# Kernel tuning notes

Measured on AMD Instinct MI355X. Metric: run time of the kernel, lower is better.

Reference implementation:

```python
import jax, jax.numpy as jnp
import numpy as np

B, N, D = 4, 2048, 1024
H, DH = 16, 64
MAX_POS_EMB = 256
TOPK = 64


def setup_inputs() -> dict:
    key = jax.random.key(0)
    ks = jax.random.split(key, 8)
    s = 0.02
    inner = H * DH
    return {
        "x": jax.random.normal(ks[0], (B, N, D), jnp.float32),
        "gating_mask": jax.random.uniform(ks[1], (B, 1, N, 1), jnp.float32),
        "Wq": jax.random.normal(ks[2], (D, inner), jnp.float32) * s,
        "bq": jnp.zeros((inner,), jnp.float32),
        "Wkv": jax.random.normal(ks[3], (D, 2 * inner), jnp.float32) * s,
        "bkv": jnp.zeros((2 * inner,), jnp.float32),
        "Wo": jax.random.normal(ks[4], (inner, D), jnp.float32) * s,
        "bo": jnp.zeros((D,), jnp.float32),
        "rel_emb": jax.random.normal(ks[5], (MAX_POS_EMB, DH), jnp.float32) * s,
        "mask": jnp.ones((B, N), bool),
        "sparse_topk": TOPK,
    }


def reference(x, gating_mask, Wq, bq, Wkv, bkv, Wo, bo, rel_emb, mask, sparse_topk):
    b, n, d = x.shape
    h, dh = H, DH
    scale = dh ** -0.5
    mask_val = -jnp.finfo(x.dtype).max

    # projections -> [b, h, n, dh]
    q = (x @ Wq + bq).reshape(b, n, h, dh).transpose(0, 2, 1, 3)
    kv = x @ Wkv + bkv
    k = kv[..., : h * dh].reshape(b, n, h, dh).transpose(0, 2, 1, 3)
    v = kv[..., h * dh:].reshape(b, n, h, dh).transpose(0, 2, 1, 3)

    dots = jnp.einsum("bhid,bhjd->bhij", q, k) * scale  # [b,h,n,n]

    # relative positional bias: q . E[clip(i-j+M, 0, M-1)]
    seq = jnp.arange(n)
    dist = jnp.clip(seq[:, None] - seq[None, :] + MAX_POS_EMB, 0, MAX_POS_EMB - 1)
    qE = jnp.einsum("bhid,rd->bhir", q, rel_emb) * scale  # [b,h,n,R]
    pos_attn = jnp.take_along_axis(qE, dist[None, None, :, :], axis=-1)  # [b,h,n,n]
    dots = dots + pos_attn

    # padding mask: mask_i * mask_j
    full_mask = mask[:, None, :, None] & mask[:, None, None, :]
    dots = jnp.where(full_mask, dots, mask_val)

    # topk sparsification: keep only scores >= k-th largest per row
    top = jax.lax.top_k(dots, sparse_topk)[0]  # [b,h,n,topk]
    vk = top[..., -1:]
    dots = jnp.where(dots < vk, mask_val, dots)

    attn = jax.nn.softmax(dots, axis=-1)
    attn = attn * gating_mask

    out = jnp.einsum("bhij,bhjd->bhid", attn, v)
    out = out.transpose(0, 2, 1, 3).reshape(b, n, h * dh)
    return out @ Wo + bo
```

## Files before the change

kernel.cpp:

```cpp
#include <hip/hip_runtime.h>
#include <stdint.h>


typedef __attribute__((ext_vector_type(8))) short short8;
typedef __attribute__((ext_vector_type(4))) float floatx4;

#define Bn   4
#define Nn   2048
#define Hn   16
#define BHn  (Bn*Hn)
#define DELTA 0.00125f

__device__ __forceinline__ float bf2f(unsigned short u) {
  union { unsigned int i; float f; } v; v.i = ((unsigned int)u) << 16; return v.f;
}
__device__ __forceinline__ unsigned short f2bf(float f) {
  union { float f; unsigned int i; } v; v.f = f;
  unsigned int r = v.i + 0x7fffu + ((v.i >> 16) & 1u);
  return (unsigned short)(r >> 16);
}
__device__ __forceinline__ floatx4 mfma16(short8 a, short8 b, floatx4 c) {
  return __builtin_amdgcn_mfma_f32_16x16x32_bf16(a, b, c, 0, 0, 0);
}
__device__ __forceinline__ void split2(float x, unsigned short& h, unsigned short& m) {
  h = f2bf(x);
  m = f2bf(x - bf2f(h));
}
__device__ __forceinline__ void split3(float x, unsigned short& h, unsigned short& m, unsigned short& l) {
  h = f2bf(x);
  float r = x - bf2f(h);
  m = f2bf(r);
  l = f2bf(r - bf2f(m));
}

__global__ __launch_bounds__(256)
void transpose_split3(const float* __restrict__ W,
                      unsigned short* __restrict__ T0,
                      unsigned short* __restrict__ T1,
                      unsigned short* __restrict__ T2,
                      int K, int Ncols)
{
  __shared__ float tile[32][33];
  int k0 = blockIdx.y * 32, n0 = blockIdx.x * 32;
  int tx = threadIdx.x & 31, ty = threadIdx.x >> 5;
  for (int s = 0; s < 32; s += 8)
    tile[ty + s][tx] = W[(size_t)(k0 + ty + s) * Ncols + n0 + tx];
  __syncthreads();
  for (int s = 0; s < 32; s += 8) {
    float x = tile[tx][ty + s];
    unsigned short h, m, l;
    split3(x, h, m, l);
    size_t o = (size_t)(n0 + ty + s) * K + k0 + tx;
    T0[o] = h; T1[o] = m; T2[o] = l;
  }
}

__global__ __launch_bounds__(256)
void transpose_split2(const float* __restrict__ W,
                      unsigned short* __restrict__ T0,
                      unsigned short* __restrict__ T1,
                      int K, int Ncols)
{
  __shared__ float tile[32][33];
  int k0 = blockIdx.y * 32, n0 = blockIdx.x * 32;
  int tx = threadIdx.x & 31, ty = threadIdx.x >> 5;
  for (int s = 0; s < 32; s += 8)
    tile[ty + s][tx] = W[(size_t)(k0 + ty + s) * Ncols + n0 + tx];
  __syncthreads();
  for (int s = 0; s < 32; s += 8) {
    float x = tile[tx][ty + s];
    unsigned short h, m;
    split2(x, h, m);
    size_t o = (size_t)(n0 + ty + s) * K + k0 + tx;
    T0[o] = h; T1[o] = m;
  }
}

__global__ __launch_bounds__(256)
void convert_bf16(const float* __restrict__ in, unsigned short* __restrict__ outp, int n) {
  int i = blockIdx.x * 256 + threadIdx.x;
  if (i < n) outp[i] = f2bf(in[i]);
}

__global__ __launch_bounds__(256)
void gemm_qkv(const float* __restrict__ A,
              const unsigned short* __restrict__ B0,
              const unsigned short* __restrict__ B1,
              const unsigned short* __restrict__ B2,
              const float* __restrict__ bias,
              float* __restrict__ O32,
              unsigned short* __restrict__ Oh,
              unsigned short* __restrict__ Om,
              _Float16* __restrict__ Vh,
              int K, float scale)
{
  __shared__ unsigned short lA[3][128 * 40];
  __shared__ unsigned short lB[3][128 * 40];
  const int tid = threadIdx.x;
  const int lane = tid & 63;
  const int m0 = blockIdx.y * 128, n0 = blockIdx.x * 128;
  const bool vblk = (n0 >= 1024);
  const int wid = tid >> 6, wm = wid >> 1, wn = wid & 1;
  const int fr = lane & 15, fq = lane >> 4;
  floatx4 acc[4][4] = {};

  for (int k0 = 0; k0 < K; k0 += 32) {
    __syncthreads();
    #pragma unroll
    for (int p = 0; p < 2; p++) {
      int c = tid + p * 256;
      int row = c >> 2, kc = (c & 3) * 8;
      size_t go = (size_t)(m0 + row) * K + k0 + kc;
      float4 v0 = *(const float4*)&A[go];
      float4 v1 = *(const float4*)&A[go + 4];
      union { unsigned short u[8]; uint4 q; } hh, mm, ll;
      float xs[8] = {v0.x, v0.y, v0.z, v0.w, v1.x, v1.y, v1.z, v1.w};
      #pragma unroll
      for (int e = 0; e < 8; e++) split3(xs[e], hh.u[e], mm.u[e], ll.u[e]);
      *(uint4*)&lA[0][row * 40 + kc] = hh.q;
      *(uint4*)&lA[1][row * 40 + kc] = mm.q;
      size_t bo = (size_t)(n0 + row) * K + k0 + kc;
      *(uint4*)&lB[0][row * 40 + kc] = *(const uint4*)&B0[bo];
      *(uint4*)&lB[1][row * 40 + kc] = *(const uint4*)&B1[bo];
      if (!vblk) {
        *(uint4*)&lA[2][row * 40 + kc] = ll.q;
        *(uint4*)&lB[2][row * 40 + kc] = *(const uint4*)&B2[bo];
      }
    }
    __syncthreads();
    short8 af0[4], af1[4], af2[4], bf0[4], bf1[4], bf2v[4];
    #pragma unroll
    for (int t = 0; t < 4; t++) {
      int ao = (wm * 64 + t * 16 + fr) * 40 + 8 * fq;
      int bo2 = (wn * 64 + t * 16 + fr) * 40 + 8 * fq;
      af0[t] = *(const short8*)&lA[0][ao];
      af1[t] = *(const short8*)&lA[1][ao];
      bf0[t] = *(const short8*)&lB[0][bo2];
      bf1[t] = *(const short8*)&lB[1][bo2];
      if (!vblk) {
        af2[t] = *(const short8*)&lA[2][ao];
        bf2v[t] = *(const short8*)&lB[2][bo2];
      }
    }
    #pragma unroll
    for (int mi = 0; mi < 4; mi++)
      #pragma unroll
      for (int ni = 0; ni < 4; ni++) {
        acc[mi][ni] = mfma16(af0[mi], bf0[ni], acc[mi][ni]);
        acc[mi][ni] = mfma16(af0[mi], bf1[ni], acc[mi][ni]);
        acc[mi][ni] = mfma16(af1[mi], bf0[ni], acc[mi][ni]);
        if (!vblk) {
          acc[mi][ni] = mfma16(af1[mi], bf1[ni], acc[mi][ni]);
          acc[mi][ni] = mfma16(af0[mi], bf2v[ni], acc[mi][ni]);
          acc[mi][ni] = mfma16(af2[mi], bf0[ni], acc[mi][ni]);
        }
      }
  }
  #pragma unroll
  for (int mi = 0; mi < 4; mi++)
    #pragma unroll
    for (int ni = 0; ni < 4; ni++) {
      int nl = n0 + wn * 64 + ni * 16 + fr;
      float bv = bias[nl];
      #pragma unroll
      for (int rg = 0; rg < 4; rg++) {
        int ml = m0 + wm * 64 + mi * 16 + fq * 4 + rg;
        float val = (acc[mi][ni][rg] + bv) * scale;
        int bb = ml >> 11, ii = ml & 2047;
        int hh2 = (nl & 1023) >> 6, dd = nl & 63;
        size_t idx = (((size_t)bb * Hn + hh2) * Nn + ii) * 64 + dd;
        if (!vblk) {
          O32[idx] = val;
          unsigned short h, m;
          split2(val, h, m);
          Oh[idx] = h; Om[idx] = m;
        } else {
          Vh[idx] = (_Float16)val;
        }
      }
    }
}

__global__ __launch_bounds__(256)
void gemm_out(const float* __restrict__ A,
              const unsigned short* __restrict__ B0,
              const unsigned short* __restrict__ B1,
              const float* __restrict__ bias,
              float* __restrict__ O32,
              int Ncols, int K)
{
  __shared__ unsigned short lA[2][128 * 40];
  __shared__ unsigned short lB[2][128 * 40];
  const int tid = threadIdx.x;
  const int lane = tid & 63;
  const int m0 = blockIdx.y * 128, n0 = blockIdx.x * 128;
  const int wid = tid >> 6, wm = wid >> 1, wn = wid & 1;
  const int fr = lane & 15, fq = lane >> 4;
  floatx4 acc[4][4] = {};

  for (int k0 = 0; k0 < K; k0 += 32) {
    __syncthreads();
    #pragma unroll
    for (int p = 0; p < 2; p++) {
      int c = tid + p * 256;
      int row = c >> 2, kc = (c & 3) * 8;
      size_t go = (size_t)(m0 + row) * K + k0 + kc;
      float4 v0 = *(const float4*)&A[go];
      float4 v1 = *(const float4*)&A[go + 4];
      union { unsigned short u[8]; uint4 q; } hh, mm;
      float xs[8] = {v0.x, v0.y, v0.z, v0.w, v1.x, v1.y, v1.z, v1.w};
      #pragma unroll
      for (int e = 0; e < 8; e++) split2(xs[e], hh.u[e], mm.u[e]);
      *(uint4*)&lA[0][row * 40 + kc] = hh.q;
      *(uint4*)&lA[1][row * 40 + kc] = mm.q;
      size_t bo = (size_t)(n0 + row) * K + k0 + kc;
      *(uint4*)&lB[0][row * 40 + kc] = *(const uint4*)&B0[bo];
      *(uint4*)&lB[1][row * 40 + kc] = *(const uint4*)&B1[bo];
    }
    __syncthreads();
    short8 af[2][4], bfr[2][4];
    #pragma unroll
    for (int s = 0; s < 2; s++)
      #pragma unroll
      for (int t = 0; t < 4; t++) {
        af[s][t]  = *(const short8*)&lA[s][(wm * 64 + t * 16 + fr) * 40 + 8 * fq];
        bfr[s][t] = *(const short8*)&lB[s][(wn * 64 + t * 16 + fr) * 40 + 8 * fq];
      }
    #pragma unroll
    for (int mi = 0; mi < 4; mi++)
      #pragma unroll
      for (int ni = 0; ni < 4; ni++) {
        acc[mi][ni] = mfma16(af[0][mi], bfr[0][ni], acc[mi][ni]);
        acc[mi][ni] = mfma16(af[0][mi], bfr[1][ni], acc[mi][ni]);
        acc[mi][ni] = mfma16(af[1][mi], bfr[0][ni], acc[mi][ni]);
      }
  }
  #pragma unroll
  for (int mi = 0; mi < 4; mi++)
    #pragma unroll
    for (int ni = 0; ni < 4; ni++) {
      int nl = n0 + wn * 64 + ni * 16 + fr;
      float bv = bias[nl];
      #pragma unroll
      for (int rg = 0; rg < 4; rg++) {
        int ml = m0 + wm * 64 + mi * 16 + fq * 4 + rg;
        O32[(size_t)ml * Ncols + nl] = acc[mi][ni][rg] + bv;
      }
    }
}

__global__ __launch_bounds__(1024, 8)
void attn_k(const unsigned short* __restrict__ qh,
            const unsigned short* __restrict__ qm,
            const unsigned short* __restrict__ kh,
            const unsigned short* __restrict__ km,
            const _Float16* __restrict__ vh,
            const float* __restrict__ q32,
            const float* __restrict__ k32,
            const unsigned short* __restrict__ relbf,
            const float* __restrict__ rel32,
            const float* __restrict__ gating,
            const int* __restrict__ topkp,
            float* __restrict__ inner)
{
  extern __shared__ char smem[];
  _Float16* S = (_Float16*)smem;
  unsigned short* KtH = (unsigned short*)(smem + 65536);
  unsigned short* KtM = KtH + 4096;
  _Float16* qE = (_Float16*)KtH;

  const int ib = blockIdx.x, bh = blockIdx.y;
  const int i0 = ib * 16;
  const int b = bh >> 4, h = bh & 15;
  const int tid = threadIdx.x;
  const int lane = tid & 63, w = tid >> 6;
  const int fr = lane & 15, fq = lane >> 4;
  const int topk = topkp[0];

  const size_t qoff = ((size_t)bh * Nn + i0) * 64;
  const size_t qf = qoff + (size_t)fr * 64 + 8 * fq;
  const short8 aqh0 = *(const short8*)&qh[qf];
  const short8 aqh1 = *(const short8*)&qh[qf + 32];
  const short8 aqm0 = *(const short8*)&qm[qf];
  const short8 aqm1 = *(const short8*)&qm[qf + 32];

  for (int jt = 0; jt < 32; jt++) {
    __syncthreads();
    {
      int sel = tid >> 9;
      int row = (tid >> 3) & 63, ch = tid & 7;
      int dst = row * 64 + ((ch ^ (row & 7)) * 8);
      size_t g = ((size_t)bh * Nn + jt * 64 + row) * 64 + ch * 8;
      unsigned short* T = sel ? KtM : KtH;
      const unsigned short* src = sel ? km : kh;
      *(uint4*)&T[dst] = *(const uint4*)&src[g];
    }
    __syncthreads();
    if (w < 8 && ((jt & 1) == (w >> 2))) {
      int wc = w & 3;
      int row16 = wc * 16 + fr, r7 = fr & 7;
      int b0 = row16 * 64 + ((fq ^ r7) * 8);
      int b1 = row16 * 64 + (((fq + 4) ^ r7) * 8);
      short8 kh0 = *(const short8*)&KtH[b0];
      short8 kh1 = *(const short8*)&KtH[b1];
      short8 km0 = *(const short8*)&KtM[b0];
      short8 km1 = *(const short8*)&KtM[b1];
      floatx4 c = {};
      c = mfma16(aqh0, kh0, c); c = mfma16(aqh1, kh1, c);
      c = mfma16(aqh0, km0, c); c = mfma16(aqh1, km1, c);
      c = mfma16(aqm0, kh0, c); c = mfma16(aqm1, kh1, c);
      int colsw = jt * 64 + ((wc ^ fq) * 16) + fr;
      #pragma unroll
      for (int rg = 0; rg < 4; rg++)
        S[(fq * 4 + rg) * 2048 + colsw] = (_Float16)c[rg];
    }
  }
  __syncthreads();

  {
    size_t rf = (size_t)(w * 16 + fr) * 64 + 8 * fq;
    short8 rb0 = *(const short8*)&relbf[rf];
    short8 rb1 = *(const short8*)&relbf[rf + 32];
    floatx4 c = {};
    c = mfma16(aqh0, rb0, c); c = mfma16(aqh1, rb1, c);
    c = mfma16(aqm0, rb0, c); c = mfma16(aqm1, rb1, c);
    int colsw = ((w ^ fq) * 16) + fr;
    #pragma unroll
    for (int rg = 0; rg < 4; rg++)
      qE[(fq * 4 + rg) * 256 + colsw] = (_Float16)c[rg];
  }
  __syncthreads();

  const int r = w;
  const int i = i0 + r;
  const int X = (r >> 2) << 4;
  _Float16* S0 = S + r * 2048;
  const _Float16* qE0 = qE + r * 256;
  const float cA = (float)qE0[255 ^ X], cC = (float)qE0[X];
  const int swl = (2 * lane) ^ X;

  float key[32];
  float mx = -3.0e38f, sm = 0.f, sq = 0.f;
  #pragma unroll
  for (int e = 0; e < 16; e++) {
    const int jb = 128 * e;
    union { unsigned int u; _Float16 hx[2]; } u0;
    u0.u = *(const unsigned int*)&S0[jb + swl];
    const int j0 = jb + 2 * lane;
    float e0, e1;
    if (jb + 127 <= i) { e0 = cA; e1 = cA; }
    else if (jb >= i + 256) { e0 = cC; e1 = cC; }
    else {
      int c0 = i - j0 + 256; c0 = c0 < 0 ? 0 : (c0 > 255 ? 255 : c0);
      int c1 = i - j0 + 255; c1 = c1 < 0 ? 0 : (c1 > 255 ? 255 : c1);
      e0 = (float)qE0[c0 ^ X]; e1 = (float)qE0[c1 ^ X];
    }
    float a0 = (float)u0.hx[0] + e0, a1 = (float)u0.hx[1] + e1;
    key[2 * e] = a0; key[2 * e + 1] = a1;
    mx = fmaxf(mx, fmaxf(a0, a1));
    sm += a0 + a1;
    sq = fmaf(a0, a0, fmaf(a1, a1, sq));
  }
  #pragma unroll
  for (int d = 1; d < 64; d <<= 1) {
    mx = fmaxf(mx, __shfl_xor(mx, d));
    sm += __shfl_xor(sm, d);
    sq += __shfl_xor(sq, d);
  }
  const float mu = sm * (1.f / 2048.f);
  const float sg = sqrtf(fmaxf(sq * (1.f / 2048.f) - mu * mu, 0.f)) + 1e-9f;

  auto cntGE = [&](float u) -> int {
    int c = 0;
    #pragma unroll
    for (int t = 0; t < 32; t++) c += (key[t] >= u) ? 1 : 0;
    #pragma unroll
    for (int d = 1; d < 64; d <<= 1) c += __shfl_xor(c, d);
    return c;
  };

  float lo = mu + 1.6f * sg;
  float hi = mx + fabsf(mx) * 1e-6f + 1e-20f;
  if (cntGE(lo) < topk) {
    lo = mu;
    if (cntGE(lo) < topk) lo = mu - 20.f * sg;
  }
  #pragma unroll 1
  for (int it = 0; it < 10; it++) {
    float mid = 0.5f * (lo + hi);
    if (cntGE(mid) >= topk) lo = mid; else hi = mid;
  }
  const float C = hi + 2.f * DELTA, L = lo - 2.f * DELTA;

  char* sb = (char*)S0;
  float* Pl = (float*)sb;          int* Jl = (int*)(sb + 512);
  float* Sx = (float*)(sb + 1024); int* Jc = (int*)(sb + 1280);
  asm volatile("" ::: "memory");
  const unsigned long long lmlt = (1ull << lane) - 1ull;

  int base = 0, mc = 0;
  #pragma unroll
  for (int t = 0; t < 32; t++) {
    const int j = 2 * lane + 128 * (t >> 1) + (t & 1);
    bool dk = key[t] >= C;
    bool cd = (key[t] >= L) && !dk;
    unsigned long long mk = __ballot(dk);
    if (dk) { int pos = base + __popcll(mk & lmlt); Pl[pos] = key[t]; Jl[pos] = j; }
    base += __popcll(mk);
    mk = __ballot(cd);
    if (cd) { int pos = mc + __popcll(mk & lmlt); if (pos < 64) Jc[pos] = j; }
    mc += __popcll(mk);
  }
  if (mc > 64) mc = 64;
  asm volatile("" ::: "memory");

  const double qv = (double)q32[((size_t)bh * Nn + i) * 64 + lane];
  #pragma unroll 1
  for (int c2 = 0; c2 < mc; c2++) {
    int j = Jc[c2];
    int ridx = i - j + 256; ridx = ridx < 0 ? 0 : (ridx > 255 ? 255 : ridx);
    double t = qv * ((double)k32[((size_t)bh * Nn + j) * 64 + lane] +
                     (double)rel32[ridx * 64 + lane]);
    #pragma unroll
    for (int d = 1; d < 64; d <<= 1) t += __shfl_xor(t, d);
    if (lane == 0) Sx[c2] = (float)t;
  }
  asm volatile("" ::: "memory");

  const int need = topk - base;
  float myx = (lane < mc) ? Sx[lane] : -3.0e38f;
  int rank = 0;
  #pragma unroll 1
  for (int c2 = 0; c2 < mc; c2++) {
    float o = Sx[c2];
    rank += (o > myx || (o == myx && c2 < lane)) ? 1 : 0;
  }
  unsigned long long bm = __ballot((lane < mc) && (rank == need - 1));
  float vk = bm ? __shfl(myx, (int)__ffsll(bm) - 1) : 3.0e38f;
  bool ck = (lane < mc) && ((rank < need) || (myx == vk));
  unsigned long long km2 = __ballot(ck);
  if (ck) { int pos = base + __popcll(km2 & lmlt); Pl[pos] = myx; Jl[pos] = Jc[lane]; }
  const int nk = base + __popcll(km2);
  asm volatile("" ::: "memory");

  float ps = 0.f;
  #pragma unroll 1
  for (int t = lane; t < nk; t += 64) { float p = __expf(Pl[t] - mx); Pl[t] = p; ps += p; }
  #pragma unroll
  for (int d = 1; d < 64; d <<= 1) ps += __shfl_xor(ps, d);
  const float coef = gating[(size_t)b * Nn + i] / ps;
  asm volatile("" ::: "memory");

  const _Float16* vbp = vh + (size_t)bh * Nn * 64 + lane;
  float a0 = 0.f, a1 = 0.f, a2 = 0.f, a3 = 0.f;
  int t4 = nk & ~3;
  #pragma unroll 1
  for (int t = 0; t < t4; t += 4) {
    float p0 = Pl[t], p1 = Pl[t + 1], p2 = Pl[t + 2], p3 = Pl[t + 3];
    int j0 = Jl[t], j1 = Jl[t + 1], j2 = Jl[t + 2], j3 = Jl[t + 3];
    a0 += p0 * (float)vbp[(size_t)j0 * 64];
    a1 += p1 * (float)vbp[(size_t)j1 * 64];
    a2 += p2 * (float)vbp[(size_t)j2 * 64];
    a3 += p3 * (float)vbp[(size_t)j3 * 64];
  }
  #pragma unroll 1
  for (int t = t4; t < nk; t++) a0 += Pl[t] * (float)vbp[(size_t)Jl[t] * 64];
  inner[((size_t)b * Nn + i) * 1024 + h * 64 + lane] = (a0 + a1 + a2 + a3) * coef;
}

extern "C" void kernel_launch(void* const* d_in, const int* in_sizes, int n_in,
                              void* d_out, int out_size, void* d_ws, size_t ws_size,
                              hipStream_t stream) {
  const float* x      = (const float*)d_in[0];
  const float* gating = (const float*)d_in[1];
  const float* Wq     = (const float*)d_in[2];
  const float* bq     = (const float*)d_in[3];
  const float* Wkv    = (const float*)d_in[4];
  const float* bkv    = (const float*)d_in[5];
  const float* Wo     = (const float*)d_in[6];
  const float* bo     = (const float*)d_in[7];
  const float* rel    = (const float*)d_in[8];
  const int*   topk   = (const int*)d_in[10];
  float* out = (float*)d_out;

  char* ws = (char*)d_ws;
  size_t off = 0;
  auto alloc = [&](size_t bytes) -> void* {
    void* p = ws + off; off += (bytes + 255) & ~(size_t)255; return p;
  };
  unsigned short* Wqt0 = (unsigned short*)alloc(1024ull * 1024 * 2);
  unsigned short* Wqt1 = (unsigned short*)alloc(1024ull * 1024 * 2);
  unsigned short* Wqt2 = (unsigned short*)alloc(1024ull * 1024 * 2);
  unsigned short* Wkt0 = (unsigned short*)alloc(2048ull * 1024 * 2);
  unsigned short* Wkt1 = (unsigned short*)alloc(2048ull * 1024 * 2);
  unsigned short* Wkt2 = (unsigned short*)alloc(2048ull * 1024 * 2);
  unsigned short* Wot0 = (unsigned short*)alloc(1024ull * 1024 * 2);
  unsigned short* Wot1 = (unsigned short*)alloc(1024ull * 1024 * 2);
  unsigned short* relbf = (unsigned short*)alloc(256ull * 64 * 2);
  float* q32 = (float*)alloc((size_t)BHn * Nn * 64 * 4);
  float* k32 = (float*)alloc((size_t)BHn * Nn * 64 * 4);
  unsigned short* qhb = (unsigned short*)alloc((size_t)BHn * Nn * 64 * 2);
  unsigned short* qmb = (unsigned short*)alloc((size_t)BHn * Nn * 64 * 2);
  unsigned short* khb = (unsigned short*)alloc((size_t)BHn * Nn * 64 * 2);
  unsigned short* kmb = (unsigned short*)alloc((size_t)BHn * Nn * 64 * 2);
  _Float16* vhb = (_Float16*)alloc((size_t)BHn * Nn * 64 * 2);
  float* inner = (float*)alloc((size_t)Bn * Nn * 1024 * 4);
  if (off > ws_size) return;

  size_t shmem = 65536 + 16384;
  (void)hipFuncSetAttribute((const void*)attn_k,
                            hipFuncAttributeMaxDynamicSharedMemorySize, (int)shmem);

  transpose_split3<<<dim3(32, 32), 256, 0, stream>>>(Wq, Wqt0, Wqt1, Wqt2, 1024, 1024);
  transpose_split3<<<dim3(64, 32), 256, 0, stream>>>(Wkv, Wkt0, Wkt1, Wkt2, 1024, 2048);
  transpose_split2<<<dim3(32, 32), 256, 0, stream>>>(Wo, Wot0, Wot1, 1024, 1024);
  convert_bf16<<<dim3(64), 256, 0, stream>>>(rel, relbf, 256 * 64);

  gemm_qkv<<<dim3(8, 64), 256, 0, stream>>>(x, Wqt0, Wqt1, Wqt2, bq,
      q32, qhb, qmb, vhb, 1024, 0.125f);
  gemm_qkv<<<dim3(16, 64), 256, 0, stream>>>(x, Wkt0, Wkt1, Wkt2, bkv,
      k32, khb, kmb, vhb, 1024, 1.0f);

  attn_k<<<dim3(128, 64), 1024, shmem, stream>>>(qhb, qmb, khb, kmb, vhb,
      q32, k32, relbf, rel, gating, topk, inner);

  gemm_out<<<dim3(8, 64), 256, 0, stream>>>(inner, Wot0, Wot1, bo,
      out, 1024, 1024);
}
```

Measured before the change: 1.174 ms.

## Presplit GEMM inputs into bf16 limbs and use integer-coded top-k threshold search

Adds a presplit kernel so x is split into three bf16 limbs once, rather than inside every GEMM tile load. q/k fp32 copies are replaced by three-limb bf16 outputs, and attention writes bf16 hi/lo limbs for the output GEMM. The top-k threshold search now runs a bisection over order-preserving fp16 integer codes packed two per register instead of float keys with mean/std bracketing. Index and code are packed together in shared memory, and the candidate margin DELTA is widened. This cuts register use and repeated conversion work, at the cost of an extra pass over x and coarser fp16-quantized keys.

New measurement: 1.365 ms. +16.2%, slower.

```diff
diff --git a/kernel.cpp b/kernel.cpp
--- a/kernel.cpp
+++ b/kernel.cpp
@@ -9,7 +9,7 @@
 #define Nn   2048
 #define Hn   16
 #define BHn  (Bn*Hn)
-#define DELTA 0.00125f
+#define DELTA 0.002f
 
 __device__ __forceinline__ float bf2f(unsigned short u) {
   union { unsigned int i; float f; } v; v.i = ((unsigned int)u) << 16; return v.f;
@@ -31,6 +31,36 @@
   float r = x - bf2f(h);
   m = f2bf(r);
   l = f2bf(r - bf2f(m));
+}
+__device__ __forceinline__ unsigned int map16(unsigned int b) {
+  return (b & 0x8000u) ? (b ^ 0xFFFFu) : (b | 0x8000u);
+}
+__device__ __forceinline__ unsigned int mapf(float f) {
+  union { _Float16 h; unsigned short s; } u; u.h = (_Float16)f;
+  return map16((unsigned int)u.s);
+}
+__device__ __forceinline__ float unmapf(unsigned int c) {
+  unsigned int b = (c & 0x8000u) ? (c ^ 0x8000u) : (c ^ 0xFFFFu);
+  union { _Float16 h; unsigned short s; } u; u.s = (unsigned short)b;
+  return (float)u.h;
+}
+
+__global__ __launch_bounds__(256)
+void presplit3(const float* __restrict__ x,
+               unsigned short* __restrict__ H,
+               unsigned short* __restrict__ M,
+               unsigned short* __restrict__ L, int n4)
+{
+  int i = blockIdx.x * 256 + threadIdx.x;
+  if (i >= n4) return;
+  float4 v = ((const float4*)x)[i];
+  union { unsigned short u[4]; uint2 q; } hh, mm, ll;
+  float xs[4] = {v.x, v.y, v.z, v.w};
+  #pragma unroll
+  for (int e = 0; e < 4; e++) split3(xs[e], hh.u[e], mm.u[e], ll.u[e]);
+  ((uint2*)H)[i] = hh.q;
+  ((uint2*)M)[i] = mm.q;
+  ((uint2*)L)[i] = ll.q;
 }
 
 __global__ __launch_bounds__(256)
@@ -83,14 +113,16 @@
 }
 
 __global__ __launch_bounds__(256)
-void gemm_qkv(const float* __restrict__ A,
+void gemm_qkv(const unsigned short* __restrict__ Ah,
+              const unsigned short* __restrict__ Am,
+              const unsigned short* __restrict__ Al,
               const unsigned short* __restrict__ B0,
               const unsigned short* __restrict__ B1,
               const unsigned short* __restrict__ B2,
               const float* __restrict__ bias,
-              float* __restrict__ O32,
               unsigned short* __restrict__ Oh,
               unsigned short* __restrict__ Om,
+              unsigned short* __restrict__ Ol,
               _Float16* __restrict__ Vh,
               int K, float scale)
 {
@@ -111,19 +143,13 @@
       int c = tid + p * 256;
       int row = c >> 2, kc = (c & 3) * 8;
       size_t go = (size_t)(m0 + row) * K + k0 + kc;
-      float4 v0 = *(const float4*)&A[go];
-      float4 v1 = *(const float4*)&A[go + 4];
-      union { unsigned short u[8]; uint4 q; } hh, mm, ll;
-      float xs[8] = {v0.x, v0.y, v0.z, v0.w, v1.x, v1.y, v1.z, v1.w};
-      #pragma unroll
-      for (int e = 0; e < 8; e++) split3(xs[e], hh.u[e], mm.u[e], ll.u[e]);
-      *(uint4*)&lA[0][row * 40 + kc] = hh.q;
-      *(uint4*)&lA[1][row * 40 + kc] = mm.q;
+      *(uint4*)&lA[0][row * 40 + kc] = *(const uint4*)&Ah[go];
+      *(uint4*)&lA[1][row * 40 + kc] = *(const uint4*)&Am[go];
       size_t bo = (size_t)(n0 + row) * K + k0 + kc;
       *(uint4*)&lB[0][row * 40 + kc] = *(const uint4*)&B0[bo];
       *(uint4*)&lB[1][row * 40 + kc] = *(const uint4*)&B1[bo];
       if (!vblk) {
-        *(uint4*)&lA[2][row * 40 + kc] = ll.q;
+        *(uint4*)&lA[2][row * 40 + kc] = *(const uint4*)&Al[go];
         *(uint4*)&lB[2][row * 40 + kc] = *(const uint4*)&B2[bo];
       }
     }
@@ -170,10 +196,9 @@
         int hh2 = (nl & 1023) >> 6, dd = nl & 63;
         size_t idx = (((size_t)bb * Hn + hh2) * Nn + ii) * 64 + dd;
         if (!vblk) {
-          O32[idx] = val;
-          unsigned short h, m;
-          split2(val, h, m);
-          Oh[idx] = h; Om[idx] = m;
+          unsigned short h, m, l;
+          split3(val, h, m, l);
+          Oh[idx] = h; Om[idx] = m; Ol[idx] = l;
         } else {
           Vh[idx] = (_Float16)val;
         }
@@ -182,7 +207,8 @@
 }
 
 __global__ __launch_bounds__(256)
-void gemm_out(const float* __restrict__ A,
+void gemm_out(const unsigned short* __restrict__ Ah,
+              const unsigned short* __restrict__ Am,
               const unsigned short* __restrict__ B0,
               const unsigned short* __restrict__ B1,
               const float* __restrict__ bias,
@@ -205,14 +231,8 @@
       int c = tid + p * 256;
       int row = c >> 2, kc = (c & 3) * 8;
       size_t go = (size_t)(m0 + row) * K + k0 + kc;
-      float4 v0 = *(const float4*)&A[go];
-      float4 v1 = *(const float4*)&A[go + 4];
-      union { unsigned short u[8]; uint4 q; } hh, mm;
-      float xs[8] = {v0.x, v0.y, v0.z, v0.w, v1.x, v1.y, v1.z, v1.w};
-      #pragma unroll
-      for (int e = 0; e < 8; e++) split2(xs[e], hh.u[e], mm.u[e]);
-      *(uint4*)&lA[0][row * 40 + kc] = hh.q;
-      *(uint4*)&lA[1][row * 40 + kc] = mm.q;
+      *(uint4*)&lA[0][row * 40 + kc] = *(const uint4*)&Ah[go];
+      *(uint4*)&lA[1][row * 40 + kc] = *(const uint4*)&Am[go];
       size_t bo = (size_t)(n0 + row) * K + k0 + kc;
       *(uint4*)&lB[0][row * 40 + kc] = *(const uint4*)&B0[bo];
       *(uint4*)&lB[1][row * 40 + kc] = *(const uint4*)&B1[bo];
@@ -252,16 +272,17 @@
 __global__ __launch_bounds__(1024, 8)
 void attn_k(const unsigned short* __restrict__ qh,
             const unsigned short* __restrict__ qm,
+            const unsigned short* __restrict__ ql,
             const unsigned short* __restrict__ kh,
             const unsigned short* __restrict__ km,
+            const unsigned short* __restrict__ kl,
             const _Float16* __restrict__ vh,
-            const float* __restrict__ q32,
-            const float* __restrict__ k32,
             const unsigned short* __restrict__ relbf,
             const float* __restrict__ rel32,
             const float* __restrict__ gating,
             const int* __restrict__ topkp,
-            float* __restrict__ inner)
+            unsigned short* __restrict__ innerh,
+            unsigned short* __restrict__ innerm)
 {
   extern __shared__ char smem[];
   _Float16* S = (_Float16*)smem;
@@ -339,8 +360,8 @@
   const float cA = (float)qE0[255 ^ X], cC = (float)qE0[X];
   const int swl = (2 * lane) ^ X;
 
-  float key[32];
-  float mx = -3.0e38f, sm = 0.f, sq = 0.f;
+  unsigned int kk[16];
+  unsigned int umax = 0;
   #pragma unroll
   for (int e = 0; e < 16; e++) {
     const int jb = 128 * e;
@@ -356,56 +377,58 @@
       e0 = (float)qE0[c0 ^ X]; e1 = (float)qE0[c1 ^ X];
     }
     float a0 = (float)u0.hx[0] + e0, a1 = (float)u0.hx[1] + e1;
-    key[2 * e] = a0; key[2 * e + 1] = a1;
-    mx = fmaxf(mx, fmaxf(a0, a1));
-    sm += a0 + a1;
-    sq = fmaf(a0, a0, fmaf(a1, a1, sq));
-  }
+    unsigned int c0u = mapf(a0), c1u = mapf(a1);
+    kk[e] = c0u | (c1u << 16);
+    unsigned int cmx = c0u > c1u ? c0u : c1u;
+    umax = umax > cmx ? umax : cmx;
+  }
+  unsigned int mxu = umax, mnu = umax;
   #pragma unroll
   for (int d = 1; d < 64; d <<= 1) {
-    mx = fmaxf(mx, __shfl_xor(mx, d));
-    sm += __shfl_xor(sm, d);
-    sq += __shfl_xor(sq, d);
-  }
-  const float mu = sm * (1.f / 2048.f);
-  const float sg = sqrtf(fmaxf(sq * (1.f / 2048.f) - mu * mu, 0.f)) + 1e-9f;
-
-  auto cntGE = [&](float u) -> int {
-    int c = 0;
-    #pragma unroll
-    for (int t = 0; t < 32; t++) c += (key[t] >= u) ? 1 : 0;
-    #pragma unroll
-    for (int d = 1; d < 64; d <<= 1) c += __shfl_xor(c, d);
-    return c;
-  };
-
-  float lo = mu + 1.6f * sg;
-  float hi = mx + fabsf(mx) * 1e-6f + 1e-20f;
-  if (cntGE(lo) < topk) {
-    lo = mu;
-    if (cntGE(lo) < topk) lo = mu - 20.f * sg;
-  }
+    unsigned int o1 = (unsigned int)__shfl_xor((int)mxu, d);
+    unsigned int o2 = (unsigned int)__shfl_xor((int)mnu, d);
+    mxu = o1 > mxu ? o1 : mxu;
+    mnu = o2 < mnu ? o2 : mnu;
+  }
+  const float mxv = unmapf(mxu);
+
+  unsigned int lo = mnu, hi = mxu + 1;
   #pragma unroll 1
-  for (int it = 0; it < 10; it++) {
-    float mid = 0.5f * (lo + hi);
-    if (cntGE(mid) >= topk) lo = mid; else hi = mid;
-  }
-  const float C = hi + 2.f * DELTA, L = lo - 2.f * DELTA;
+  for (int it = 0; it < 13; it++) {
+    unsigned int mid = (lo + hi) >> 1;
+    int cnt = 0;
+    #pragma unroll
+    for (int e = 0; e < 16; e++) {
+      cnt += ((kk[e] & 0xffffu) >= mid) ? 1 : 0;
+      cnt += ((kk[e] >> 16) >= mid) ? 1 : 0;
+    }
+    #pragma unroll
+    for (int d = 1; d < 64; d <<= 1) cnt += __shfl_xor(cnt, d);
+    if (cnt >= topk) lo = mid; else hi = mid;
+  }
+  const float Cv = unmapf(hi) + 2.0f * DELTA;
+  const float Lv = unmapf(lo) - 2.0f * DELTA;
+  const unsigned int Cu = mapf(Cv) + 1;
+  int Lsi = (int)mapf(Lv) - 1;
+  const unsigned int Lu = Lsi < 0 ? 0u : (unsigned int)Lsi;
 
   char* sb = (char*)S0;
-  float* Pl = (float*)sb;          int* Jl = (int*)(sb + 512);
-  float* Sx = (float*)(sb + 1024); int* Jc = (int*)(sb + 1280);
+  unsigned int* Pk = (unsigned int*)sb;
+  int*   Jc = (int*)(sb + 512);
+  float* Sx = (float*)(sb + 768);
+  float* P2 = (float*)(sb + 1024);
   asm volatile("" ::: "memory");
   const unsigned long long lmlt = (1ull << lane) - 1ull;
 
   int base = 0, mc = 0;
   #pragma unroll
   for (int t = 0; t < 32; t++) {
+    unsigned int code = (t & 1) ? (kk[t >> 1] >> 16) : (kk[t >> 1] & 0xffffu);
     const int j = 2 * lane + 128 * (t >> 1) + (t & 1);
-    bool dk = key[t] >= C;
-    bool cd = (key[t] >= L) && !dk;
+    bool dk = code >= Cu;
+    bool cd = (code >= Lu) && !dk;
     unsigned long long mk = __ballot(dk);
-    if (dk) { int pos = base + __popcll(mk & lmlt); Pl[pos] = key[t]; Jl[pos] = j; }
+    if (dk) { int pos = base + __popcll(mk & lmlt); Pk[pos] = (unsigned int)j | (code << 16); }
     base += __popcll(mk);
     mk = __ballot(cd);
     if (cd) { int pos = mc + __popcll(mk & lmlt); if (pos < 64) Jc[pos] = j; }
@@ -414,16 +437,18 @@
   if (mc > 64) mc = 64;
   asm volatile("" ::: "memory");
 
-  const double qv = (double)q32[((size_t)bh * Nn + i) * 64 + lane];
+  const size_t qrow = ((size_t)bh * Nn + i) * 64 + lane;
+  const double qv = (double)bf2f(qh[qrow]) + (double)bf2f(qm[qrow]) + (double)bf2f(ql[qrow]);
   #pragma unroll 1
   for (int c2 = 0; c2 < mc; c2++) {
     int j = Jc[c2];
     int ridx = i - j + 256; ridx = ridx < 0 ? 0 : (ridx > 255 ? 255 : ridx);
-    double t = qv * ((double)k32[((size_t)bh * Nn + j) * 64 + lane] +
-                     (double)rel32[ridx * 64 + lane]);
-    #pragma unroll
-    for (int d = 1; d < 64; d <<= 1) t += __shfl_xor(t, d);
-    if (lane == 0) Sx[c2] = (float)t;
+    size_t krow = ((size_t)bh * Nn + j) * 64 + lane;
+    double kv = (double)bf2f(kh[krow]) + (double)bf2f(km[krow]) + (double)bf2f(kl[krow]);
+    double t2 = qv * (kv + (double)rel32[ridx * 64 + lane]);
+    #pragma unroll
+    for (int d = 1; d < 64; d <<= 1) t2 += __shfl_xor(t2, d);
+    if (lane == 0) Sx[c2] = (float)t2;
   }
   asm volatile("" ::: "memory");
 
@@ -439,13 +464,21 @@
   float vk = bm ? __shfl(myx, (int)__ffsll(bm) - 1) : 3.0e38f;
   bool ck = (lane < mc) && ((rank < need) || (myx == vk));
   unsigned long long km2 = __ballot(ck);
-  if (ck) { int pos = base + __popcll(km2 & lmlt); Pl[pos] = myx; Jl[pos] = Jc[lane]; }
+  float pb = 0.f;
+  if (ck) {
+    int pos = base + __popcll(km2 & lmlt);
+    Pk[pos] = (unsigned int)Jc[lane];
+    pb = __expf(myx - mxv);
+    P2[pos] = pb;
+  }
   const int nk = base + __popcll(km2);
-  asm volatile("" ::: "memory");
-
-  float ps = 0.f;
+  float ps = pb;
   #pragma unroll 1
-  for (int t = lane; t < nk; t += 64) { float p = __expf(Pl[t] - mx); Pl[t] = p; ps += p; }
+  for (int t = lane; t < base; t += 64) {
+    float val = unmapf(Pk[t] >> 16);
+    float p = __expf(val - mxv);
+    P2[t] = p; ps += p;
+  }
   #pragma unroll
   for (int d = 1; d < 64; d <<= 1) ps += __shfl_xor(ps, d);
   const float coef = gating[(size_t)b * Nn + i] / ps;
@@ -456,16 +489,22 @@
   int t4 = nk & ~3;
   #pragma unroll 1
   for (int t = 0; t < t4; t += 4) {
-    float p0 = Pl[t], p1 = Pl[t + 1], p2 = Pl[t + 2], p3 = Pl[t + 3];
-    int j0 = Jl[t], j1 = Jl[t + 1], j2 = Jl[t + 2], j3 = Jl[t + 3];
+    int j0 = (int)(Pk[t] & 0xffffu), j1 = (int)(Pk[t + 1] & 0xffffu);
+    int j2 = (int)(Pk[t + 2] & 0xffffu), j3 = (int)(Pk[t + 3] & 0xffffu);
+    float p0 = P2[t], p1 = P2[t + 1], p2 = P2[t + 2], p3 = P2[t + 3];
     a0 += p0 * (float)vbp[(size_t)j0 * 64];
     a1 += p1 * (float)vbp[(size_t)j1 * 64];
     a2 += p2 * (float)vbp[(size_t)j2 * 64];
     a3 += p3 * (float)vbp[(size_t)j3 * 64];
   }
   #pragma unroll 1
-  for (int t = t4; t < nk; t++) a0 += Pl[t] * (float)vbp[(size_t)Jl[t] * 64];
-  inner[((size_t)b * Nn + i) * 1024 + h * 64 + lane] = (a0 + a1 + a2 + a3) * coef;
+  for (int t = t4; t < nk; t++)
+    a0 += P2[t] * (float)vbp[(size_t)(Pk[t] & 0xffffu) * 64];
+  float outv = (a0 + a1 + a2 + a3) * coef;
+  unsigned short oh, om;
+  split2(outv, oh, om);
+  size_t oidx = ((size_t)b * Nn + i) * 1024 + h * 64 + lane;
+  innerh[oidx] = oh; innerm[oidx] = om;
 }
 
 extern "C" void kernel_launch(void* const* d_in, const int* in_sizes, int n_in,
@@ -497,33 +536,38 @@
   unsigned short* Wot0 = (unsigned short*)alloc(1024ull * 1024 * 2);
   unsigned short* Wot1 = (unsigned short*)alloc(1024ull * 1024 * 2);
   unsigned short* relbf = (unsigned short*)alloc(256ull * 64 * 2);
-  float* q32 = (float*)alloc((size_t)BHn * Nn * 64 * 4);
-  float* k32 = (float*)alloc((size_t)BHn * Nn * 64 * 4);
+  unsigned short* xh = (unsigned short*)alloc(8192ull * 1024 * 2);
+  unsigned short* xm = (unsigned short*)alloc(8192ull * 1024 * 2);
+  unsigned short* xl = (unsigned short*)alloc(8192ull * 1024 * 2);
   unsigned short* qhb = (unsigned short*)alloc((size_t)BHn * Nn * 64 * 2);
   unsigned short* qmb = (unsigned short*)alloc((size_t)BHn * Nn * 64 * 2);
+  unsigned short* qlb = (unsigned short*)alloc((size_t)BHn * Nn * 64 * 2);
   unsigned short* khb = (unsigned short*)alloc((size_t)BHn * Nn * 64 * 2);
   unsigned short* kmb = (unsigned short*)alloc((size_t)BHn * Nn * 64 * 2);
+  unsigned short* klb = (unsigned short*)alloc((size_t)BHn * Nn * 64 * 2);
   _Float16* vhb = (_Float16*)alloc((size_t)BHn * Nn * 64 * 2);
-  float* inner = (float*)alloc((size_t)Bn * Nn * 1024 * 4);
+  unsigned short* innerh = (unsigned short*)alloc((size_t)Bn * Nn * 1024 * 2);
+  unsigned short* innerm = (unsigned short*)alloc((size_t)Bn * Nn * 1024 * 2);
   if (off > ws_size) return;
 
   size_t shmem = 65536 + 16384;
   (void)hipFuncSetAttribute((const void*)attn_k,
                             hipFuncAttributeMaxDynamicSharedMemorySize, (int)shmem);
 
+  presplit3<<<dim3(8192), 256, 0, stream>>>(x, xh, xm, xl, 8192 * 1024 / 4);
   transpose_split3<<<dim3(32, 32), 256, 0, stream>>>(Wq, Wqt0, Wqt1, Wqt2, 1024, 1024);
   transpose_split3<<<dim3(64, 32), 256, 0, stream>>>(Wkv, Wkt0, Wkt1, Wkt2, 1024, 2048);
   transpose_split2<<<dim3(32, 32), 256, 0, stream>>>(Wo, Wot0, Wot1, 1024, 1024);
   convert_bf16<<<dim3(64), 256, 0, stream>>>(rel, relbf, 256 * 64);
 
-  gemm_qkv<<<dim3(8, 64), 256, 0, stream>>>(x, Wqt0, Wqt1, Wqt2, bq,
-      q32, qhb, qmb, vhb, 1024, 0.125f);
-  gemm_qkv<<<dim3(16, 64), 256, 0, stream>>>(x, Wkt0, Wkt1, Wkt2, bkv,
-      k32, khb, kmb, vhb, 1024, 1.0f);
-
-  attn_k<<<dim3(128, 64), 1024, shmem, stream>>>(qhb, qmb, khb, kmb, vhb,
-      q32, k32, relbf, rel, gating, topk, inner);
-
-  gemm_out<<<dim3(8, 64), 256, 0, stream>>>(inner, Wot0, Wot1, bo,
+  gemm_qkv<<<dim3(8, 64), 256, 0, stream>>>(xh, xm, xl, Wqt0, Wqt1, Wqt2, bq,
+      qhb, qmb, qlb, vhb, 1024, 0.125f);
+  gemm_qkv<<<dim3(16, 64), 256, 0, stream>>>(xh, xm, xl, Wkt0, Wkt1, Wkt2, bkv,
+      khb, kmb, klb, vhb, 1024, 1.0f);
+
+  attn_k<<<dim3(128, 64), 1024, shmem, stream>>>(qhb, qmb, qlb, khb, kmb, klb,
+      vhb, relbf, rel, gating, topk, innerh, innerm);
+
+  gemm_out<<<dim3(8, 64), 256, 0, stream>>>(innerh, innerm, Wot0, Wot1, bo,
       out, 1024, 1024);
 }
```
